# Optimization experiments

Hardware: AMD Instinct MI355X
Metric: run time of the kernel (lower is better)

Reference implementation:

```python
import jax, jax.numpy as jnp
import numpy as np
from jax import lax

B, H, W, CIN = 16, 224, 224, 8
F = 256            # filter_inpt feature dim
K = 3              # ksize (square)
NC = 16            # n_channels (output channels)
NP = CIN * NC * K * K  # 1152 dynamic filter params per sample


def setup_inputs() -> dict:
    key = jax.random.key(0)
    ks = jax.random.split(key, 8)
    s_in = 1.0 / np.sqrt(F)
    return {
        "inpt": jax.random.normal(ks[0], (B, H, W, CIN), jnp.float32),
        "filter_inpt": jax.random.normal(ks[1], (B, F), jnp.float32),
        # param_layer_1 (ELU affine, F -> F)
        "W1": jax.random.normal(ks[2], (F, F), jnp.float32) * s_in,
        "b1": jnp.zeros((F,), jnp.float32),
        # dynamic_weights affine (F -> NP), uniform_unit_scaling(0.1)-like scale
        "Wd": jax.random.normal(ks[3], (F, NP), jnp.float32) * (0.1 * s_in),
        "bd": jnp.zeros((NP,), jnp.float32),
        # dynamic_bias affine (F -> NC), scale sqrt(2)
        "Wb": jax.random.normal(ks[4], (F, NC), jnp.float32) * (np.sqrt(2.0) * s_in),
        "bb": jnp.zeros((NC,), jnp.float32),
        # static learned bias (1,1,1,NC)
        "dfn_bias": jax.random.normal(ks[5], (1, 1, 1, NC), jnp.float32) * 0.01,
    }


def reference(inpt, filter_inpt, W1, b1, Wd, bd, Wb, bb, dfn_bias):
    # param layers: (n_param_layers - 1) = 1 ELU affine keeping width F
    h = jax.nn.elu(filter_inpt @ W1 + b1)                      # [B, F]
    dyn = h @ Wd + bd                                          # [B, CIN*NC*K*K]
    # per-sample filter, ordered (Cin, kh, kw, out_ch) to match patch layout below
    w = dyn.reshape(B, CIN * K * K, NC)                        # [B, P, NC]
    # im2col patches: conv_general_dilated_patches on NCHW -> [B, CIN*K*K, H, W]
    patches = lax.conv_general_dilated_patches(
        jnp.transpose(inpt, (0, 3, 1, 2)), (K, K), (1, 1), 'SAME')
    patches = jnp.transpose(patches, (0, 2, 3, 1))             # [B, H, W, P]
    out = jnp.einsum('bhwp,bpc->bhwc', patches, w)             # [B, H, W, NC]
    # adaptive (per-sample) bias + static bias
    out = out + (h @ Wb + bb)[:, None, None, :] + dfn_bias
    return jax.nn.elu(out)
```

## Files before the change

### kernel.cpp

```cpp
#include <hip/hip_runtime.h>
#include <math.h>

constexpr int BN  = 16;
constexpr int HH  = 224;
constexpr int WW  = 224;
constexpr int CI  = 8;
constexpr int FF  = 256;
constexpr int NC  = 16;
constexpr int NP  = 1152;

typedef __attribute__((ext_vector_type(8))) short short8;
typedef __attribute__((ext_vector_type(4))) float f32x4;

__device__ __forceinline__ float elu_f(float x) {
    return x > 0.0f ? x : (__expf(x) - 1.0f);
}

__device__ __forceinline__ void split8(const float* v, short8& hi, short8& lo) {
#pragma unroll
    for (int j = 0; j < 8; ++j) {
        const unsigned u = __float_as_uint(v[j]);
        hi[j] = (short)(u >> 16);
        const float hf = __uint_as_float(u & 0xffff0000u);
        lo[j] = (short)(__float_as_uint(v[j] - hf) >> 16);
    }
}

__global__ __launch_bounds__(128) void k_h(const float* __restrict__ fi,
                                           const float* __restrict__ W1,
                                           const float* __restrict__ b1,
                                           const float* __restrict__ bd,
                                           const float* __restrict__ bb,
                                           const float* __restrict__ dfn,
                                           float* __restrict__ hp,
                                           float* __restrict__ w_out,
                                           float* __restrict__ bias_out) {
    __shared__ float x[64];
    const int bid  = blockIdx.x;
    const int b    = bid >> 3;
    const int half = (bid >> 2) & 1;
    const int ks   = bid & 3;
    const int t    = threadIdx.x;

    if (t < 64) x[t] = fi[b * FF + ks * 64 + t];
    __syncthreads();

    const int col = half * 128 + t;
    float acc = (ks == 0) ? b1[col] : 0.0f;
#pragma unroll 8
    for (int k = 0; k < 64; ++k)
        acc = fmaf(x[k], W1[(ks * 64 + k) * FF + col], acc);
    hp[(ks * BN + b) * FF + col] = acc;

    const int gid = bid * 128 + t;
    for (int i = gid; i < BN * NP; i += 16384) {
        const int c = i - (i / NP) * NP;
        w_out[i] = bd[c];
    }
    if (gid < BN * NC) bias_out[gid] = bb[gid & 15] + dfn[gid & 15];
}

__global__ __launch_bounds__(128) void k_dyn(const float* __restrict__ hp,
                                             const float* __restrict__ Wd,
                                             const float* __restrict__ Wb,
                                             float* __restrict__ w_out,
                                             float* __restrict__ bias_out) {
    __shared__ float hs[16][32];
    const int bid = blockIdx.x;
    const int cg  = bid % 9;
    const int ks  = bid / 9;
    const int k0  = ks * 32;
    const int t   = threadIdx.x;

#pragma unroll
    for (int j = 0; j < 4; ++j) {
        const int idx = t + 128 * j;
        const int bi = idx >> 5, kk = idx & 31;
        const int o = bi * FF + k0 + kk;
        const float s = hp[o] + hp[BN * FF + o] +
                        hp[2 * BN * FF + o] + hp[3 * BN * FF + o];
        hs[bi][kk] = elu_f(s);
    }
    __syncthreads();

    const int i = cg * 128 + t;
    float a[16];
#pragma unroll
    for (int b = 0; b < 16; ++b) a[b] = 0.0f;

#pragma unroll 8
    for (int kk = 0; kk < 32; ++kk) {
        const float w = Wd[(size_t)(k0 + kk) * NP + i];
#pragma unroll
        for (int b = 0; b < 16; ++b) a[b] = fmaf(hs[b][kk], w, a[b]);
    }
#pragma unroll
    for (int b = 0; b < 16; ++b) atomicAdd(&w_out[b * NP + i], a[b]);

    if (cg == 0) {
#pragma unroll
        for (int r = 0; r < 2; ++r) {
            const int p = t + r * 128;
            const int b = p >> 4, c = p & 15;
            float s = 0.0f;
#pragma unroll 8
            for (int kk = 0; kk < 32; ++kk)
                s = fmaf(hs[b][kk], Wb[(size_t)(k0 + kk) * NC + c], s);
            atomicAdd(&bias_out[b * NC + c], s);
        }
    }
}

__global__ __launch_bounds__(128) void k_conv(const float* __restrict__ in,
                                              const float* __restrict__ w_all,
                                              const float* __restrict__ bias_all,
                                              float* __restrict__ out) {
    const int b    = blockIdx.z;
    const int half = blockIdx.x;
    const int t    = threadIdx.x;
    const int wid  = t >> 6;
    const int lane = t & 63;
    const int cl   = lane & 15;
    const int g    = lane >> 4;
    const int y    = blockIdx.y * 2 + wid;

    int  dyL[3], dxL[3];
    bool real[3];
#pragma unroll
    for (int c = 0; c < 3; ++c) {
        const int tap = c * 4 + g;
        real[c] = (tap < 9);
        const int tp = real[c] ? tap : 0;
        dyL[c] = tp / 3;
        dxL[c] = tp - 3 * dyL[c];
    }

    const float* __restrict__ wq = w_all + b * NP;
    short8 bhi0, blo0, bhi1, blo1, bhi2, blo2;
    {
        float wv[8];
#pragma unroll
        for (int i = 0; i < 8; ++i)
            wv[i] = real[0] ? wq[(i * 9 + (0 * 4 + g)) * NC + cl] : 0.0f;
        split8(wv, bhi0, blo0);
#pragma unroll
        for (int i = 0; i < 8; ++i)
            wv[i] = real[1] ? wq[(i * 9 + (1 * 4 + g)) * NC + cl] : 0.0f;
        split8(wv, bhi1, blo1);
#pragma unroll
        for (int i = 0; i < 8; ++i)
            wv[i] = real[2] ? wq[(i * 9 + (2 * 4 + g)) * NC + cl] : 0.0f;
        split8(wv, bhi2, blo2);
    }

    size_t ro[3];
    bool   okr[3];
#pragma unroll
    for (int c = 0; c < 3; ++c) {
        const int iy = y + dyL[c] - 1;
        okr[c] = real[c] && ((unsigned)iy < (unsigned)HH);
        const int iyc = min(max(iy, 0), HH - 1);
        ro[c] = ((size_t)(b * HH + iyc) * WW) * CI;
    }

    const float bias = bias_all[b * NC + cl];
    const size_t orow = ((size_t)(b * HH + y) * WW) * NC;

#pragma unroll 1
    for (int tx = 0; tx < 7; ++tx) {
        const int x0 = (half * 7 + tx) * 16;
        f32x4 accM = {bias, bias, bias, bias};
        f32x4 accL = {0.f, 0.f, 0.f, 0.f};
        f32x4 accH = {0.f, 0.f, 0.f, 0.f};

#pragma unroll
        for (int c = 0; c < 3; ++c) {
            const int  ix = x0 + cl + dxL[c] - 1;
            const bool ok = okr[c] && ((unsigned)ix < (unsigned)WW);
            const int  ixc = min(max(ix, 0), WW - 1);
            const float4* pp = (const float4*)(in + ro[c] + (size_t)ixc * CI);
            const float4 a0 = pp[0];
            const float4 a1 = pp[1];
            float av[8];
            av[0] = ok ? a0.x : 0.0f;
            av[1] = ok ? a0.y : 0.0f;
            av[2] = ok ? a0.z : 0.0f;
            av[3] = ok ? a0.w : 0.0f;
            av[4] = ok ? a1.x : 0.0f;
            av[5] = ok ? a1.y : 0.0f;
            av[6] = ok ? a1.z : 0.0f;
            av[7] = ok ? a1.w : 0.0f;
            short8 ahi, alo;
            split8(av, ahi, alo);
            const short8 bh = (c == 0) ? bhi0 : (c == 1) ? bhi1 : bhi2;
            const short8 bl = (c == 0) ? blo0 : (c == 1) ? blo1 : blo2;
            accM = __builtin_amdgcn_mfma_f32_16x16x32_bf16(ahi, bh, accM, 0, 0, 0);
            accL = __builtin_amdgcn_mfma_f32_16x16x32_bf16(alo, bh, accL, 0, 0, 0);
            accH = __builtin_amdgcn_mfma_f32_16x16x32_bf16(ahi, bl, accH, 0, 0, 0);
        }

#pragma unroll
        for (int r = 0; r < 4; ++r) {
            const int px = g * 4 + r;
            out[orow + (size_t)(x0 + px) * NC + cl] =
                elu_f(accM[r] + accL[r] + accH[r]);
        }
    }
}

extern "C" void kernel_launch(void* const* d_in, const int* in_sizes, int n_in,
                              void* d_out, int out_size, void* d_ws, size_t ws_size,
                              hipStream_t stream) {
    const float* inpt = (const float*)d_in[0];
    const float* fi   = (const float*)d_in[1];
    const float* W1   = (const float*)d_in[2];
    const float* b1   = (const float*)d_in[3];
    const float* Wd   = (const float*)d_in[4];
    const float* bd   = (const float*)d_in[5];
    const float* Wb   = (const float*)d_in[6];
    const float* bb   = (const float*)d_in[7];
    const float* dfn  = (const float*)d_in[8];
    float* out = (float*)d_out;

    float* ws    = (float*)d_ws;
    float* hp    = ws;
    float* wDyn  = ws + 16384;
    float* biasA = ws + 16384 + 18432;

    k_h  <<<128, 128, 0, stream>>>(fi, W1, b1, bd, bb, dfn, hp, wDyn, biasA);
    k_dyn<<<72, 128, 0, stream>>>(hp, Wd, Wb, wDyn, biasA);
    k_conv<<<dim3(2, 112, BN), 128, 0, stream>>>(inpt, wDyn, biasA, out);
}
```

Measured before the change: 40.04 us.

## Stage input halo tile in LDS and transpose MFMA for vectorized stores

The conv kernel now loads a 4-row by 114-column halo tile of the input into shared memory once per block. The bf16 hi/lo split is done once per pixel there rather than for every one of the nine taps that reuse it. The MFMA operands are swapped so each lane holds four consecutive output channels for one pixel, allowing a single float4 store per lane instead of four scalar stores. This adds an LDS footprint of about 14.8KB and a block barrier, while reducing redundant global loads and split arithmetic.

```diff
diff --git a/kernel.cpp b/kernel.cpp
--- a/kernel.cpp
+++ b/kernel.cpp
@@ -115,6 +115,8 @@
                                               const float* __restrict__ w_all,
                                               const float* __restrict__ bias_all,
                                               float* __restrict__ out) {
+    __shared__ short8 lsA[4][116][2];
+
     const int b    = blockIdx.z;
     const int half = blockIdx.x;
     const int t    = threadIdx.x;
@@ -122,7 +124,30 @@
     const int lane = t & 63;
     const int cl   = lane & 15;
     const int g    = lane >> 4;
-    const int y    = blockIdx.y * 2 + wid;
+    const int yb0  = blockIdx.y * 2;
+    const int xb0  = half * 112;
+
+    for (int s = t; s < 456; s += 128) {
+        const int r  = s / 114;
+        const int j  = s - r * 114;
+        const int gy = yb0 - 1 + r;
+        const int gx = xb0 - 1 + j;
+        const bool ok = ((unsigned)gy < (unsigned)HH) &&
+                        ((unsigned)gx < (unsigned)WW);
+        float av[8] = {0.f, 0.f, 0.f, 0.f, 0.f, 0.f, 0.f, 0.f};
+        if (ok) {
+            const float4* pp =
+                (const float4*)(in + ((size_t)(b * HH + gy) * WW + gx) * CI);
+            const float4 a0 = pp[0];
+            const float4 a1 = pp[1];
+            av[0] = a0.x; av[1] = a0.y; av[2] = a0.z; av[3] = a0.w;
+            av[4] = a1.x; av[5] = a1.y; av[6] = a1.z; av[7] = a1.w;
+        }
+        short8 hi, lo;
+        split8(av, hi, lo);
+        lsA[r][j][0] = hi;
+        lsA[r][j][1] = lo;
+    }
 
     int  dyL[3], dxL[3];
     bool real[3];
@@ -153,58 +178,38 @@
         split8(wv, bhi2, blo2);
     }
 
-    size_t ro[3];
-    bool   okr[3];
-#pragma unroll
-    for (int c = 0; c < 3; ++c) {
-        const int iy = y + dyL[c] - 1;
-        okr[c] = real[c] && ((unsigned)iy < (unsigned)HH);
-        const int iyc = min(max(iy, 0), HH - 1);
-        ro[c] = ((size_t)(b * HH + iyc) * WW) * CI;
-    }
-
-    const float bias = bias_all[b * NC + cl];
+    __syncthreads();
+
+    const float4 bias4 = ((const float4*)(bias_all + b * NC))[g];
+    const int y = yb0 + wid;
     const size_t orow = ((size_t)(b * HH + y) * WW) * NC;
 
 #pragma unroll 1
     for (int tx = 0; tx < 7; ++tx) {
-        const int x0 = (half * 7 + tx) * 16;
-        f32x4 accM = {bias, bias, bias, bias};
+        const int x0 = xb0 + tx * 16;
+        f32x4 accM = {bias4.x, bias4.y, bias4.z, bias4.w};
         f32x4 accL = {0.f, 0.f, 0.f, 0.f};
         f32x4 accH = {0.f, 0.f, 0.f, 0.f};
 
 #pragma unroll
         for (int c = 0; c < 3; ++c) {
-            const int  ix = x0 + cl + dxL[c] - 1;
-            const bool ok = okr[c] && ((unsigned)ix < (unsigned)WW);
-            const int  ixc = min(max(ix, 0), WW - 1);
-            const float4* pp = (const float4*)(in + ro[c] + (size_t)ixc * CI);
-            const float4 a0 = pp[0];
-            const float4 a1 = pp[1];
-            float av[8];
-            av[0] = ok ? a0.x : 0.0f;
-            av[1] = ok ? a0.y : 0.0f;
-            av[2] = ok ? a0.z : 0.0f;
-            av[3] = ok ? a0.w : 0.0f;
-            av[4] = ok ? a1.x : 0.0f;
-            av[5] = ok ? a1.y : 0.0f;
-            av[6] = ok ? a1.z : 0.0f;
-            av[7] = ok ? a1.w : 0.0f;
-            short8 ahi, alo;
-            split8(av, ahi, alo);
+            const int j = tx * 16 + cl + dxL[c];
+            const int r = wid + dyL[c];
+            const short8 ahi = lsA[r][j][0];
+            const short8 alo = lsA[r][j][1];
             const short8 bh = (c == 0) ? bhi0 : (c == 1) ? bhi1 : bhi2;
             const short8 bl = (c == 0) ? blo0 : (c == 1) ? blo1 : blo2;
-            accM = __builtin_amdgcn_mfma_f32_16x16x32_bf16(ahi, bh, accM, 0, 0, 0);
-            accL = __builtin_amdgcn_mfma_f32_16x16x32_bf16(alo, bh, accL, 0, 0, 0);
-            accH = __builtin_amdgcn_mfma_f32_16x16x32_bf16(ahi, bl, accH, 0, 0, 0);
+            accM = __builtin_amdgcn_mfma_f32_16x16x32_bf16(bh, ahi, accM, 0, 0, 0);
+            accL = __builtin_amdgcn_mfma_f32_16x16x32_bf16(bh, alo, accL, 0, 0, 0);
+            accH = __builtin_amdgcn_mfma_f32_16x16x32_bf16(bl, ahi, accH, 0, 0, 0);
         }
 
-#pragma unroll
-        for (int r = 0; r < 4; ++r) {
-            const int px = g * 4 + r;
-            out[orow + (size_t)(x0 + px) * NC + cl] =
-                elu_f(accM[r] + accL[r] + accH[r]);
-        }
+        float4 res;
+        res.x = elu_f(accM[0] + accL[0] + accH[0]);
+        res.y = elu_f(accM[1] + accL[1] + accH[1]);
+        res.z = elu_f(accM[2] + accL[2] + accH[2]);
+        res.w = elu_f(accM[3] + accL[3] + accH[3]);
+        ((float4*)(out + orow + (size_t)(x0 + cl) * NC))[g] = res;
     }
 }
 
```

Result: no change. 39.73 us (-0.8%).
